# Optimization experiments

Hardware: AMD Instinct MI355X
Metric: run time of the kernel (lower is better)

Reference implementation:

```python
import jax, jax.numpy as jnp
import numpy as np

L, B, D = 50, 1024, 512      # memory slots, batch, d_model
H, DK = 4, 512               # heads, per-head dim (d_k = d_model in this module)
HOP = 3


def setup_inputs() -> dict:
    key = jax.random.key(0)
    ks = jax.random.split(key, 16)
    s = lambda i, shape: jax.random.normal(ks[i], shape, jnp.float32) * 0.02
    return dict(
        momery=jax.random.normal(ks[0], (L, B, D), jnp.float32),
        hid=jax.random.normal(ks[1], (B, D), jnp.float32),
        text_polarity=jax.random.normal(ks[2], (B,), jnp.float32),
        attribute_polarity=jax.random.normal(ks[3], (B,), jnp.float32),
        w=jnp.array(0.5, jnp.float32),
        p_w1=s(4, (D, D)), p_b1=jnp.zeros((D,), jnp.float32),
        p_w2=s(5, (D, D)), p_b2=jnp.zeros((D,), jnp.float32),
        wq=s(6, (D, H * DK)), bq=jnp.zeros((H * DK,), jnp.float32),
        wk=s(7, (D, H * DK)), bk=jnp.zeros((H * DK,), jnp.float32),
        wv=s(8, (D, H * DK)), bv=jnp.zeros((H * DK,), jnp.float32),
        wo=s(9, (H * DK, D)), bo=jnp.zeros((D,), jnp.float32),
    )


def reference(momery, hid, text_polarity, attribute_polarity, w,
              p_w1, p_b1, p_w2, p_b2, wq, bq, wk, bk, wv, bv, wo, bo):
    # k, v depend only on hid (attinkv = hid every hop/slot) -> hoist out of hop loop
    k = (hid @ wk + bk).reshape(B, H, DK)   # [B,H,DK]
    v = (hid @ wv + bv).reshape(B, H, DK)   # [B,H,DK]
    inv_sqrt_dk = jnp.float32(1.0 / np.sqrt(DK))
    for _ in range(HOP):
        # projection MLP over all slots at once (replaces per-slot loop)
        mid = jax.nn.relu(momery @ p_w1 + p_b1) @ p_w2 + p_b2          # [L,B,D]
        q = (mid @ wq + bq).reshape(L, B, H, DK)                        # [L,B,H,DK]
        # single key per query (nk=1): scores [L,B,H,1], softmax -> ones
        scores = (jnp.einsum('lbhd,bhd->lbh', q, k) * inv_sqrt_dk)[..., None]
        att = jax.nn.softmax(scores, axis=-1)                           # [L,B,H,1]
        out = att * v                                                   # [L,B,H,DK]
        temp = out.reshape(L, B, H * DK) @ wo + bo                      # [L,B,D]
        momery = momery + w * temp
    return momery
```

## Files before the change

### kernel.cpp

```cpp
#include <hip/hip_runtime.h>
#include <hip/hip_bf16.h>

typedef short short8 __attribute__((ext_vector_type(8)));
typedef float f4 __attribute__((ext_vector_type(4)));

__device__ __forceinline__ short f2bfs(float f) {
    __hip_bfloat16 h = __float2bfloat16(f);
    return __builtin_bit_cast(short, h);
}

__device__ __forceinline__ unsigned packbf2(float a, float b, float s) {
    unsigned lo = (unsigned short)f2bfs(s * a);
    unsigned hi = (unsigned short)f2bfs(s * b);
    return (hi << 16) | lo;
}

#define MFMA(a, b, c) __builtin_amdgcn_mfma_f32_16x16x32_bf16(a, b, c, 0, 0, 0)

__global__ __launch_bounds__(256) void gemmW(const float* __restrict__ wv,
                                             const float* __restrict__ wo,
                                             const float* __restrict__ bv,
                                             const float* __restrict__ w,
                                             short* __restrict__ WsT,
                                             float* __restrict__ b2p) {
    constexpr int K = 2048, N = 512, NT = 16;
    const int tid = threadIdx.x;
    const int bx  = blockIdx.x;

    if (bx >= 256) {
        const int jb = bx - 256;
        const float* pv = bv + jb * 512;
#pragma unroll
        for (int cc = 0; cc < 2; ++cc) {
            const int c = tid + cc * 256;
            const float* pw = wo + (size_t)(jb * 512) * N + c;
            float s = 0.f;
#pragma unroll 8
            for (int j = 0; j < 512; ++j) s += pv[j] * pw[(size_t)j * N];
            b2p[jb * 512 + c] = s;
        }
        return;
    }

    __shared__ float red[4][32][33];

    const int row0 = (bx >> 4) * 32;
    const int col0 = (bx & 15) * 32;
    const int lane = tid & 63, wave = tid >> 6;
    const int ln = lane & 15, q = lane >> 4;
    const int k0 = wave * 512;

    const float* pa0 = wv + (size_t)(row0 + ln) * K + k0 + q * 8;
    const float* pa1 = pa0 + (size_t)16 * K;
    const float* pb  = wo + (size_t)(k0 + q * 8) * N;

    float4 a00 = *(const float4*)pa0, a01 = *(const float4*)(pa0 + 4);
    float4 a10 = *(const float4*)pa1, a11 = *(const float4*)(pa1 + 4);
    float b0r[8], b1r[8];
#pragma unroll
    for (int j = 0; j < 8; ++j) {
        b0r[j] = pb[(size_t)j * N + col0 + ln];
        b1r[j] = pb[(size_t)j * N + col0 + 16 + ln];
    }

    f4 acc00 = {0,0,0,0}, acc01 = {0,0,0,0}, acc10 = {0,0,0,0}, acc11 = {0,0,0,0};

    for (int t = 0; t < NT; ++t) {
        short8 af0, af1, bf0, bf1;
        af0[0]=f2bfs(a00.x); af0[1]=f2bfs(a00.y); af0[2]=f2bfs(a00.z); af0[3]=f2bfs(a00.w);
        af0[4]=f2bfs(a01.x); af0[5]=f2bfs(a01.y); af0[6]=f2bfs(a01.z); af0[7]=f2bfs(a01.w);
        af1[0]=f2bfs(a10.x); af1[1]=f2bfs(a10.y); af1[2]=f2bfs(a10.z); af1[3]=f2bfs(a10.w);
        af1[4]=f2bfs(a11.x); af1[5]=f2bfs(a11.y); af1[6]=f2bfs(a11.z); af1[7]=f2bfs(a11.w);
#pragma unroll
        for (int j = 0; j < 8; ++j) { bf0[j] = f2bfs(b0r[j]); bf1[j] = f2bfs(b1r[j]); }

        if (t + 1 < NT) {
            pa0 += 32; pa1 += 32; pb += (size_t)32 * N;
            a00 = *(const float4*)pa0; a01 = *(const float4*)(pa0 + 4);
            a10 = *(const float4*)pa1; a11 = *(const float4*)(pa1 + 4);
#pragma unroll
            for (int j = 0; j < 8; ++j) {
                b0r[j] = pb[(size_t)j * N + col0 + ln];
                b1r[j] = pb[(size_t)j * N + col0 + 16 + ln];
            }
        }
        acc00 = MFMA(af0, bf0, acc00); acc01 = MFMA(af0, bf1, acc01);
        acc10 = MFMA(af1, bf0, acc10); acc11 = MFMA(af1, bf1, acc11);
    }

#pragma unroll
    for (int r = 0; r < 4; ++r) {
        red[wave][q * 4 + r][ln]           = acc00[r];
        red[wave][q * 4 + r][ln + 16]      = acc01[r];
        red[wave][16 + q * 4 + r][ln]      = acc10[r];
        red[wave][16 + q * 4 + r][ln + 16] = acc11[r];
    }
    __syncthreads();

    const float wsc = 3.0f * w[0];
    const int n  = tid >> 3;
    const int d0 = (tid & 7) * 4;
    float s0 = red[0][d0][n]     + red[1][d0][n]     + red[2][d0][n]     + red[3][d0][n];
    float s1 = red[0][d0 + 1][n] + red[1][d0 + 1][n] + red[2][d0 + 1][n] + red[3][d0 + 1][n];
    float s2 = red[0][d0 + 2][n] + red[1][d0 + 2][n] + red[2][d0 + 2][n] + red[3][d0 + 2][n];
    float s3 = red[0][d0 + 3][n] + red[1][d0 + 3][n] + red[2][d0 + 3][n] + red[3][d0 + 3][n];
    short* p = WsT + (size_t)(col0 + n) * 512 + row0 + d0;
    *(unsigned*)p       = packbf2(s0, s1, wsc);
    *(unsigned*)(p + 2) = packbf2(s2, s3, wsc);
}

__global__ __launch_bounds__(256) void gemmT(const float* __restrict__ hid,
                                             const short* __restrict__ WsT,
                                             const float* __restrict__ b2p,
                                             const float* __restrict__ bo,
                                             const float* __restrict__ w,
                                             float* __restrict__ t) {
    constexpr int K = 512, N = 512, NT = 16;
    const int tid  = threadIdx.x;
    const int col0 = blockIdx.x * 64;
    const int row0 = blockIdx.y * 32;
    const int lane = tid & 63, wave = tid >> 6;
    const int ln = lane & 15, q = lane >> 4;
    const int col = col0 + wave * 16 + ln;

    const float* pa0 = hid + (size_t)(row0 + ln) * K + q * 8;
    const float* pa1 = pa0 + (size_t)16 * K;
    const short* pb  = WsT + (size_t)col * K + q * 8;

    float4 a00 = *(const float4*)pa0, a01 = *(const float4*)(pa0 + 4);
    float4 a10 = *(const float4*)pa1, a11 = *(const float4*)(pa1 + 4);
    short8 bf = *(const short8*)pb;

    f4 acc0 = {0,0,0,0}, acc1 = {0,0,0,0};

    for (int tt = 0; tt < NT; ++tt) {
        short8 af0, af1;
        af0[0]=f2bfs(a00.x); af0[1]=f2bfs(a00.y); af0[2]=f2bfs(a00.z); af0[3]=f2bfs(a00.w);
        af0[4]=f2bfs(a01.x); af0[5]=f2bfs(a01.y); af0[6]=f2bfs(a01.z); af0[7]=f2bfs(a01.w);
        af1[0]=f2bfs(a10.x); af1[1]=f2bfs(a10.y); af1[2]=f2bfs(a10.z); af1[3]=f2bfs(a10.w);
        af1[4]=f2bfs(a11.x); af1[5]=f2bfs(a11.y); af1[6]=f2bfs(a11.z); af1[7]=f2bfs(a11.w);
        short8 b = bf;
        if (tt + 1 < NT) {
            pa0 += 32; pa1 += 32; pb += 32;
            a00 = *(const float4*)pa0; a01 = *(const float4*)(pa0 + 4);
            a10 = *(const float4*)pa1; a11 = *(const float4*)(pa1 + 4);
            bf = *(const short8*)pb;
        }
        acc0 = MFMA(af0, b, acc0);
        acc1 = MFMA(af1, b, acc1);
    }

    const float wsc  = 3.0f * w[0];
    const float bias = wsc * (b2p[col] + b2p[512 + col] + b2p[1024 + col] +
                              b2p[1536 + col] + bo[col]);
#pragma unroll
    for (int r = 0; r < 4; ++r) {
        t[(size_t)(row0 + q * 4 + r) * N + col]      = acc0[r] + bias;
        t[(size_t)(row0 + 16 + q * 4 + r) * N + col] = acc1[r] + bias;
    }
}

__global__ __launch_bounds__(256) void bcast(const float* __restrict__ mem,
                                             const float* __restrict__ t,
                                             float* __restrict__ out) {
    constexpr int P = 131072;
    const int id  = blockIdx.x * 256 + threadIdx.x;
    const int bd4 = id & (P - 1);
    const int grp = id >> 17;
    const f4 tv = ((const f4*)t)[bd4];
    const f4* mp = (const f4*)mem + (size_t)grp * 5 * P + bd4;
    f4*       op = (f4*)out       + (size_t)grp * 5 * P + bd4;
#pragma unroll
    for (int j = 0; j < 5; ++j) {
        f4 m = __builtin_nontemporal_load(mp + (size_t)j * P);
        __builtin_nontemporal_store(m + tv, op + (size_t)j * P);
    }
}

extern "C" void kernel_launch(void* const* d_in, const int* in_sizes, int n_in,
                              void* d_out, int out_size, void* d_ws, size_t ws_size,
                              hipStream_t stream) {
    const float* momery = (const float*)d_in[0];
    const float* hid    = (const float*)d_in[1];
    const float* w      = (const float*)d_in[4];
    const float* wv     = (const float*)d_in[13];
    const float* bv     = (const float*)d_in[14];
    const float* wo     = (const float*)d_in[15];
    const float* bo     = (const float*)d_in[16];
    float* out = (float*)d_out;

    short* WsT = (short*)d_ws;
    float* b2p = (float*)(WsT + 262144);
    float* t   = b2p + 2048;

    gemmW<<<260, 256, 0, stream>>>(wv, wo, bv, w, WsT, b2p);
    gemmT<<<dim3(8, 32), 256, 0, stream>>>(hid, WsT, b2p, bo, w, t);
    bcast<<<5120, 256, 0, stream>>>(momery, t, out);
}
```

Measured before the change: 280.4 us.

## Split bias GEMV across more blocks and flatten broadcast-add kernel

The bias product bv·wo is now split over 64 extra blocks, each covering 64 rows for 512 columns, instead of 4 blocks each doing a 512-long serial loop. bo is folded into the first partial, and gemmT sums the 32 partials through shared memory. The broadcast-add kernel now uses one float4 per thread across 25600 blocks with ordinary loads and stores, replacing 5 strided nontemporal accesses per thread. The aim is to cut the serial tail of the bias blocks and raise memory-level parallelism, at the cost of more blocks launched and dropping the nontemporal hints.

```diff
diff --git a/kernel.cpp b/kernel.cpp
--- a/kernel.cpp
+++ b/kernel.cpp
@@ -20,6 +20,7 @@
 __global__ __launch_bounds__(256) void gemmW(const float* __restrict__ wv,
                                              const float* __restrict__ wo,
                                              const float* __restrict__ bv,
+                                             const float* __restrict__ bo,
                                              const float* __restrict__ w,
                                              short* __restrict__ WsT,
                                              float* __restrict__ b2p) {
@@ -28,17 +29,14 @@
     const int bx  = blockIdx.x;
 
     if (bx >= 256) {
-        const int jb = bx - 256;
-        const float* pv = bv + jb * 512;
-#pragma unroll
-        for (int cc = 0; cc < 2; ++cc) {
-            const int c = tid + cc * 256;
-            const float* pw = wo + (size_t)(jb * 512) * N + c;
-            float s = 0.f;
+        const int g = (bx - 256) * 256 + tid;
+        const int o = g & 511;
+        const int r = g >> 9;
+        float s = (r == 0) ? bo[o] : 0.f;
+        const int j0 = r * 64;
 #pragma unroll 8
-            for (int j = 0; j < 512; ++j) s += pv[j] * pw[(size_t)j * N];
-            b2p[jb * 512 + c] = s;
-        }
+        for (int j = j0; j < j0 + 64; ++j) s += bv[j] * wo[(size_t)j * N + o];
+        b2p[r * 512 + o] = s;
         return;
     }
 
@@ -112,16 +110,23 @@
 __global__ __launch_bounds__(256) void gemmT(const float* __restrict__ hid,
                                              const short* __restrict__ WsT,
                                              const float* __restrict__ b2p,
-                                             const float* __restrict__ bo,
                                              const float* __restrict__ w,
                                              float* __restrict__ t) {
     constexpr int K = 512, N = 512, NT = 16;
+    __shared__ float bred[4][64];
+
     const int tid  = threadIdx.x;
     const int col0 = blockIdx.x * 64;
     const int row0 = blockIdx.y * 32;
     const int lane = tid & 63, wave = tid >> 6;
     const int ln = lane & 15, q = lane >> 4;
     const int col = col0 + wave * 16 + ln;
+
+    const int cl = tid & 63, rr = tid >> 6;
+    const float* bpp = b2p + (size_t)(rr * 8) * 512 + col0 + cl;
+    float bp = 0.f;
+#pragma unroll
+    for (int k = 0; k < 8; ++k) bp += bpp[(size_t)k * 512];
 
     const float* pa0 = hid + (size_t)(row0 + ln) * K + q * 8;
     const float* pa1 = pa0 + (size_t)16 * K;
@@ -150,9 +155,12 @@
         acc1 = MFMA(af1, b, acc1);
     }
 
+    bred[rr][cl] = bp;
+    __syncthreads();
+    const int lc = wave * 16 + ln;
     const float wsc  = 3.0f * w[0];
-    const float bias = wsc * (b2p[col] + b2p[512 + col] + b2p[1024 + col] +
-                              b2p[1536 + col] + bo[col]);
+    const float bias = wsc * (bred[0][lc] + bred[1][lc] + bred[2][lc] + bred[3][lc]);
+
 #pragma unroll
     for (int r = 0; r < 4; ++r) {
         t[(size_t)(row0 + q * 4 + r) * N + col]      = acc0[r] + bias;
@@ -163,18 +171,11 @@
 __global__ __launch_bounds__(256) void bcast(const float* __restrict__ mem,
                                              const float* __restrict__ t,
                                              float* __restrict__ out) {
-    constexpr int P = 131072;
-    const int id  = blockIdx.x * 256 + threadIdx.x;
-    const int bd4 = id & (P - 1);
-    const int grp = id >> 17;
+    const size_t idx = (size_t)blockIdx.x * 256 + threadIdx.x;
+    const int bd4 = (int)(idx & (131072 - 1));
     const f4 tv = ((const f4*)t)[bd4];
-    const f4* mp = (const f4*)mem + (size_t)grp * 5 * P + bd4;
-    f4*       op = (f4*)out       + (size_t)grp * 5 * P + bd4;
-#pragma unroll
-    for (int j = 0; j < 5; ++j) {
-        f4 m = __builtin_nontemporal_load(mp + (size_t)j * P);
-        __builtin_nontemporal_store(m + tv, op + (size_t)j * P);
-    }
+    const f4 m  = ((const f4*)mem)[idx];
+    ((f4*)out)[idx] = m + tv;
 }
 
 extern "C" void kernel_launch(void* const* d_in, const int* in_sizes, int n_in,
@@ -191,9 +192,9 @@
 
     short* WsT = (short*)d_ws;
     float* b2p = (float*)(WsT + 262144);
-    float* t   = b2p + 2048;
-
-    gemmW<<<260, 256, 0, stream>>>(wv, wo, bv, w, WsT, b2p);
-    gemmT<<<dim3(8, 32), 256, 0, stream>>>(hid, WsT, b2p, bo, w, t);
-    bcast<<<5120, 256, 0, stream>>>(momery, t, out);
-}
+    float* t   = b2p + 32 * 512;
+
+    gemmW<<<320, 256, 0, stream>>>(wv, wo, bv, bo, w, WsT, b2p);
+    gemmT<<<dim3(8, 32), 256, 0, stream>>>(hid, WsT, b2p, w, t);
+    bcast<<<25600, 256, 0, stream>>>(momery, t, out);
+}
```

Result: faster. 241.4 us (-13.9%).
